# Performance work log

Hardware: AMD Instinct MI355X
Metric: run time of the kernel (lower is better)

The kernel has to match this reference:

```python
import jax, jax.numpy as jnp
import numpy as np

DIM = 1024
HEADS = 16
HEAD_DIM = DIM // HEADS
SCALE = HEAD_DIM ** -0.5


def setup_inputs() -> dict:
    key = jax.random.key(0)
    ks = jax.random.split(key, 9)
    b, n, m = 4, 1024, 1024
    x = jax.random.normal(ks[0], (b, n, DIM), dtype=jnp.float32)
    context = jax.random.normal(ks[1], (b, m, DIM), dtype=jnp.float32)
    mask = jax.random.randint(ks[2], (b, n, 32, 32), 0, 2, dtype=jnp.int32)
    s = DIM ** -0.5
    Wq = jax.random.normal(ks[3], (DIM, DIM), dtype=jnp.float32) * s
    bq = jnp.zeros((DIM,), dtype=jnp.float32)
    Wkv = jax.random.normal(ks[4], (DIM, 2 * DIM), dtype=jnp.float32) * s
    bkv = jnp.zeros((2 * DIM,), dtype=jnp.float32)
    Wp = jax.random.normal(ks[5], (DIM, DIM), dtype=jnp.float32) * s
    bp = jnp.zeros((DIM,), dtype=jnp.float32)
    return {"x": x, "context": context, "mask": mask,
            "Wq": Wq, "bq": bq, "Wkv": Wkv, "bkv": bkv, "Wp": Wp, "bp": bp}


def reference(x, context, mask, Wq, bq, Wkv, bkv, Wp, bp):
    b, n, _ = x.shape
    m = context.shape[1]
    h, d = HEADS, HEAD_DIM
    # projections
    q = (x @ Wq + bq).reshape(b, n, h, d).transpose(0, 2, 1, 3)       # [b,h,n,d]
    kv = (context @ Wkv + bkv).reshape(b, m, 2, h, d)
    k = kv[:, :, 0].transpose(0, 2, 1, 3)                              # [b,h,m,d]
    v = kv[:, :, 1].transpose(0, 2, 1, 3)                              # [b,h,m,d]
    dots = jnp.einsum('bhnd,bhmd->bhnm', q, k) * SCALE                 # [b,h,n,m]
    # mask: [b,n,H,W] -> [b,1,n,m]; masked_fill where mask == 0
    mflat = mask.reshape(b, n, m)[:, None]                             # [b,1,n,m]
    dots = jnp.where(mflat == 0, -jnp.inf, dots)
    attn = jax.nn.softmax(dots, axis=-1)
    out = jnp.einsum('bhnm,bhmd->bhnd', attn, v)
    out = out.transpose(0, 2, 1, 3).reshape(b, n, h * d)
    return out @ Wp + bp
```

## Files before the change

kernel.cpp:

```cpp
#include <hip/hip_runtime.h>

typedef __bf16 bf16;
typedef __bf16 bf16x8 __attribute__((ext_vector_type(8)));
typedef __bf16 bf16x4 __attribute__((ext_vector_type(4)));
typedef float f32x4 __attribute__((ext_vector_type(4)));
typedef unsigned long long u64;

#define MFMA16(a, b, c) __builtin_amdgcn_mfma_f32_16x16x32_bf16(a, b, c, 0, 0, 0)

__device__ __forceinline__ void gl_lds16(const void* g, void* l) {
  __builtin_amdgcn_global_load_lds(
      (const __attribute__((address_space(1))) unsigned int*)g,
      (__attribute__((address_space(3))) unsigned int*)l, 16, 0, 0);
}

template <int N>
__device__ __forceinline__ void wait_vmcnt() {
  asm volatile("s_waitcnt vmcnt(%0)" ::"n"(N) : "memory");
}

__device__ __forceinline__ void bar() {
  asm volatile("" ::: "memory");
  __builtin_amdgcn_s_barrier();
  asm volatile("" ::: "memory");
}

__device__ __forceinline__ float hw_exp2(float x) {
#if __has_builtin(__builtin_amdgcn_exp2f)
  return __builtin_amdgcn_exp2f(x);
#else
  float r;
  asm("v_exp_f32 %0, %1" : "=v"(r) : "v"(x));
  return r;
#endif
}

__global__ __launch_bounds__(256)
void prep_k(const float* __restrict__ Wq, const float* __restrict__ Wkv,
            const float* __restrict__ Wp, const int* __restrict__ mask,
            const float* __restrict__ context, const float* __restrict__ x,
            bf16* __restrict__ BqkvT, bf16* __restrict__ WpT,
            u64* __restrict__ maskbits, bf16* __restrict__ cb,
            bf16* __restrict__ xb) {
  const int bx = blockIdx.x;
  const int tid = threadIdx.x;
  if (bx >= 3328) {
    const size_t i = ((size_t)(bx - 3328) * 256 + tid) * 8;
    f32x4 a0 = *(const f32x4*)(x + i);
    f32x4 a1 = *(const f32x4*)(x + i + 4);
    bf16x8 t;
#pragma unroll
    for (int j = 0; j < 4; ++j) { t[j] = (bf16)a0[j]; t[4 + j] = (bf16)a1[j]; }
    *(bf16x8*)(xb + i) = t;
    return;
  }
  if (bx >= 1280) {
    const size_t i = ((size_t)(bx - 1280) * 256 + tid) * 8;
    f32x4 a0 = *(const f32x4*)(context + i);
    f32x4 a1 = *(const f32x4*)(context + i + 4);
    bf16x8 t;
#pragma unroll
    for (int j = 0; j < 4; ++j) { t[j] = (bf16)a0[j]; t[4 + j] = (bf16)a1[j]; }
    *(bf16x8*)(cb + i) = t;
    return;
  }
  if (bx >= 1024) {
    const int idx = (bx - 1024) * 256 + tid;
    const int4* p = (const int4*)(mask + (size_t)idx * 64);
    u64 v = 0;
#pragma unroll
    for (int i = 0; i < 16; ++i) {
      int4 m = p[i];
      v |= (u64)(m.x != 0) << (4 * i);
      v |= (u64)(m.y != 0) << (4 * i + 1);
      v |= (u64)(m.z != 0) << (4 * i + 2);
      v |= (u64)(m.w != 0) << (4 * i + 3);
    }
    maskbits[idx] = v;
    return;
  }
  const int ct = bx >> 4, rt = bx & 15;
  const float* src;
  bf16* dst;
  int C, c0, drow0;
  if (ct < 16) {
    src = Wq; C = 1024; c0 = ct * 64; dst = BqkvT; drow0 = c0;
  } else if (ct < 48) {
    src = Wkv; C = 2048; c0 = (ct - 16) * 64; dst = BqkvT; drow0 = 1024 + c0;
  } else {
    src = Wp; C = 1024; c0 = (ct - 48) * 64; dst = WpT; drow0 = c0;
  }
  __shared__ bf16 T[64][72];
  const int r0 = rt * 64;
#pragma unroll
  for (int i = 0; i < 2; ++i) {
    int c = i * 256 + tid;
    int row = c >> 3, col = (c & 7) * 8;
    const float* sp = &src[(size_t)(r0 + row) * C + c0 + col];
    f32x4 a0 = *(const f32x4*)sp;
    f32x4 a1 = *(const f32x4*)(sp + 4);
    bf16x8 t;
#pragma unroll
    for (int j = 0; j < 4; ++j) { t[j] = (bf16)a0[j]; t[4 + j] = (bf16)a1[j]; }
    *(bf16x8*)&T[row][col] = t;
  }
  __syncthreads();
#pragma unroll
  for (int i = 0; i < 2; ++i) {
    int c = i * 256 + tid;
    int orow = c >> 3, ocol = (c & 7) * 8;
    bf16x8 v;
#pragma unroll
    for (int j = 0; j < 8; ++j) v[j] = T[ocol + j][orow];
    *(bf16x8*)&dst[(size_t)(drow0 + orow) * 1024 + r0 + ocol] = v;
  }
}

template <int EPI, int BN>
__global__ __launch_bounds__(256, BN == 128 ? 3 : 4)
void gemm_p3(const bf16* __restrict__ A0, const bf16* __restrict__ A1,
             const bf16* __restrict__ Bt, const float* __restrict__ bias0,
             const float* __restrict__ bias1, bf16* __restrict__ oq,
             bf16* __restrict__ ok, bf16* __restrict__ ovt,
             float* __restrict__ outf) {
  constexpr int NJ = BN / 32;
  constexpr int S = 2 + BN / 64;
  __shared__ bf16 As[3][128][32];
  __shared__ bf16 Bs[3][BN][32];
  const int tid = threadIdx.x;
  const int lane = tid & 63;
  const int w = tid >> 6;
  const int wm = (w >> 1) * 64;
  const int wn = (w & 1) * (BN / 2);
  const int l15 = lane & 15, l4 = lane >> 4;
  const int lrow = lane >> 2;
  const int lcg = (lane & 3) ^ ((lrow >> 1) & 3);
  const int rdc = (l4 ^ ((l15 >> 1) & 3)) * 8;
  const int m0 = blockIdx.x * 128;
  const int n0 = blockIdx.y * BN;

  const bf16* Asrc = (EPI == 1) ? ((n0 < 1024) ? A0 : A1) : A0;

  float bc[NJ];
#pragma unroll
  for (int j = 0; j < NJ; ++j) {
    const int col = n0 + wn + j * 16 + l15;
    if (EPI == 1) bc[j] = (col < 1024) ? bias0[col] : bias1[col - 1024];
    else bc[j] = bias0[col];
  }

  f32x4 acc[4][NJ] = {};

#define STAGE(kk, buf)                                                        \
  {                                                                           \
    _Pragma("unroll") for (int it = 0; it < 2; ++it) {                        \
      const int r = w * 32 + it * 16;                                         \
      gl_lds16(&Asrc[(size_t)(m0 + r + lrow) * 1024 + (kk) + lcg * 8],        \
               &As[buf][r][0]);                                               \
    }                                                                         \
    _Pragma("unroll") for (int it = 0; it < BN / 64; ++it) {                  \
      const int r = w * (BN / 4) + it * 16;                                   \
      gl_lds16(&Bt[(size_t)(n0 + r + lrow) * 1024 + (kk) + lcg * 8],          \
               &Bs[buf][r][0]);                                               \
    }                                                                         \
  }

#define COMPUTE(buf)                                                          \
  {                                                                           \
    bf16x8 af[4], bfr[NJ];                                                    \
    _Pragma("unroll") for (int i = 0; i < 4; ++i) af[i] =                     \
        *(const bf16x8*)&As[buf][wm + i * 16 + l15][rdc];                     \
    _Pragma("unroll") for (int j = 0; j < NJ; ++j) bfr[j] =                   \
        *(const bf16x8*)&Bs[buf][wn + j * 16 + l15][rdc];                     \
    _Pragma("unroll") for (int i = 0; i < 4; ++i)                             \
        _Pragma("unroll") for (int j = 0; j < NJ; ++j) acc[i][j] =            \
            MFMA16(af[i], bfr[j], acc[i][j]);                                 \
  }

  STAGE(0, 0);
  STAGE(32, 1);
#pragma unroll 3
  for (int k = 0; k < 30; ++k) {
    wait_vmcnt<S>();
    bar();
    STAGE((k + 2) * 32, (k + 2) % 3);
    COMPUTE(k % 3);
  }
  wait_vmcnt<S>();
  bar();
  COMPUTE(0);
  wait_vmcnt<0>();
  bar();
  COMPUTE(1);
#undef STAGE
#undef COMPUTE

  const float SCALE2 = 0.18033688011112042f;
#pragma unroll
  for (int j = 0; j < NJ; ++j) {
    const int col = n0 + wn + j * 16 + l15;
#pragma unroll
    for (int i = 0; i < 4; ++i) {
#pragma unroll
      for (int r = 0; r < 4; ++r) {
        const int row = m0 + wm + i * 16 + l4 * 4 + r;
        const float v = acc[i][j][r] + bc[j];
        if (EPI == 0) {
          outf[(size_t)row * 1024 + col] = v;
        } else {
          const int b = row >> 10, n = row & 1023;
          if (col < 1024) {
            const int h = col >> 6, d = col & 63;
            oq[(((size_t)(b * 16 + h)) * 1024 + n) * 64 + d] =
                (bf16)(v * SCALE2);
          } else {
            const int ckv = col - 1024;
            const int s = ckv >> 10, c2 = ckv & 1023;
            const int h = c2 >> 6, d = c2 & 63;
            if (s == 0)
              ok[(((size_t)(b * 16 + h)) * 1024 + n) * 64 + d] = (bf16)v;
            else
              ovt[(((size_t)(b * 16 + h)) * 64 + d) * 1024 + n] = (bf16)v;
          }
        }
      }
    }
  }
}

__global__ __launch_bounds__(256, 2)
void attn_kernel(const bf16* __restrict__ q, const bf16* __restrict__ k,
                 const bf16* __restrict__ vT, const u64* __restrict__ maskbits,
                 bf16* __restrict__ ao) {
  const int bh = blockIdx.x;
  const int ntile = blockIdx.y;
  const int b = bh >> 4, h = bh & 15;
  const int tid = threadIdx.x;
  const int lane = tid & 63;
  const int w = tid >> 6;
  const int l15 = lane & 15, l4 = lane >> 4;

  __shared__ bf16 Ks[2][64][64];
  __shared__ bf16 Vts[2][64][64];
  __shared__ bf16 Pw[4][32][64];

  const size_t base = (size_t)bh * 65536;
  const int nrow0 = ntile * 128 + w * 32;

  bf16x8 qf[2][2];
#pragma unroll
  for (int f = 0; f < 2; ++f)
#pragma unroll
    for (int ks = 0; ks < 2; ++ks)
      qf[f][ks] = *(const bf16x8*)&q[base +
                                     (size_t)(nrow0 + f * 16 + l15) * 64 +
                                     ks * 32 + l4 * 8];

  const u64* mb = maskbits + (size_t)(b * 1024 + nrow0 + l15) * 16;

  const int srow = lane >> 3;
  const int sgl = (lane & 7) ^ srow;
  const bf16* kp = &k[base + (size_t)(w * 16 + srow) * 64 + sgl * 8];
  const bf16* vp = &vT[base + (size_t)(w * 16 + srow) * 1024 + sgl * 8];

  const int rc0 = ((0 + l4) ^ (l15 & 7)) * 8;
  const int rc1 = ((4 + l4) ^ (l15 & 7)) * 8;

  const int sh0 = l4 * 4;
  const int sh1 = 16 + l4 * 4;

  f32x4 o[2][4] = {};
  float lsum[2] = {0.0f, 0.0f};

#define STAGEA(mt_, buf_)                                                     \
  {                                                                           \
    _Pragma("unroll") for (int it = 0; it < 2; ++it) {                        \
      gl_lds16(kp + (size_t)((mt_)*64 + it * 8) * 64,                         \
               &Ks[buf_][w * 16 + it * 8][0]);                                \
      gl_lds16(vp + (size_t)(it * 8) * 1024 + (mt_)*64,                       \
               &Vts[buf_][w * 16 + it * 8][0]);                               \
    }                                                                         \
  }

  STAGEA(0, 0);
  u64 wm0 = mb[0];
  u64 wm1 = mb[256];
  for (int mt = 0; mt < 16; ++mt) {
    const int cur = mt & 1;
    __syncthreads();
    if (mt < 15) STAGEA(mt + 1, cur ^ 1);
    u64 nm0 = 0, nm1 = 0;
    if (mt < 15) {
      nm0 = mb[mt + 1];
      nm1 = mb[256 + mt + 1];
    }

    f32x4 s[2][4];
    __builtin_amdgcn_s_setprio(1);
#pragma unroll
    for (int sub = 0; sub < 4; ++sub) {
      bf16x8 kf0 = *(const bf16x8*)&Ks[cur][sub * 16 + l15][rc0];
      bf16x8 kf1 = *(const bf16x8*)&Ks[cur][sub * 16 + l15][rc1];
      s[0][sub] = MFMA16(kf0, qf[0][0], (f32x4)0.0f);
      s[0][sub] = MFMA16(kf1, qf[0][1], s[0][sub]);
      s[1][sub] = MFMA16(kf0, qf[1][0], (f32x4)0.0f);
      s[1][sub] = MFMA16(kf1, qf[1][1], s[1][sub]);
    }
    __builtin_amdgcn_s_setprio(0);

#pragma unroll
    for (int f = 0; f < 2; ++f) {
      const u64 wmt = f ? wm1 : wm0;
      const unsigned mlo = (unsigned)wmt;
      const unsigned mhi = (unsigned)(wmt >> 32);
#pragma unroll
      for (int sub = 0; sub < 4; ++sub) {
        const unsigned word = (sub < 2) ? mlo : mhi;
        const unsigned nib = (word >> ((sub & 1) ? sh1 : sh0)) & 15u;
        float p[4];
#pragma unroll
        for (int r = 0; r < 4; ++r) {
          float e = hw_exp2(s[f][sub][r]);
          p[r] = ((nib >> r) & 1u) ? e : 0.0f;
        }
        lsum[f] += (p[0] + p[1]) + (p[2] + p[3]);
        bf16x4 pv;
#pragma unroll
        for (int r = 0; r < 4; ++r) pv[r] = (bf16)p[r];
        const int gw = sub * 2 + (l4 >> 1);
        char* pd = (char*)&Pw[w][f * 16 + l15][0] +
                   ((gw ^ (l15 & 7)) * 16 + (l4 & 1) * 8);
        *(bf16x4*)pd = pv;
      }
    }

    bf16x8 af[2][2];
#pragma unroll
    for (int f = 0; f < 2; ++f) {
      af[f][0] = *(const bf16x8*)&Pw[w][f * 16 + l15][rc0];
      af[f][1] = *(const bf16x8*)&Pw[w][f * 16 + l15][rc1];
    }
    __builtin_amdgcn_s_setprio(1);
#pragma unroll
    for (int sub = 0; sub < 4; ++sub) {
      bf16x8 vf0 = *(const bf16x8*)&Vts[cur][sub * 16 + l15][rc0];
      bf16x8 vf1 = *(const bf16x8*)&Vts[cur][sub * 16 + l15][rc1];
      o[0][sub] = MFMA16(af[0][0], vf0, o[0][sub]);
      o[0][sub] = MFMA16(af[0][1], vf1, o[0][sub]);
      o[1][sub] = MFMA16(af[1][0], vf0, o[1][sub]);
      o[1][sub] = MFMA16(af[1][1], vf1, o[1][sub]);
    }
    __builtin_amdgcn_s_setprio(0);

    wm0 = nm0;
    wm1 = nm1;
  }
#undef STAGEA

  float inv[2][4];
#pragma unroll
  for (int f = 0; f < 2; ++f) {
    float t = lsum[f];
    t += __shfl_xor(t, 16);
    t += __shfl_xor(t, 32);
#pragma unroll
    for (int r = 0; r < 4; ++r) inv[f][r] = 1.0f / __shfl(t, l4 * 4 + r);
  }

#pragma unroll
  for (int f = 0; f < 2; ++f) {
#pragma unroll
    for (int sub = 0; sub < 4; ++sub) {
#pragma unroll
      for (int r = 0; r < 4; ++r) {
        const int n = nrow0 + f * 16 + l4 * 4 + r;
        const size_t idx =
            ((size_t)(b * 1024 + n)) * 1024 + h * 64 + sub * 16 + l15;
        ao[idx] = (bf16)(o[f][sub][r] * inv[f][r]);
      }
    }
  }
}

extern "C" void kernel_launch(void* const* d_in, const int* in_sizes, int n_in,
                              void* d_out, int out_size, void* d_ws,
                              size_t ws_size, hipStream_t stream) {
  const float* x = (const float*)d_in[0];
  const float* context = (const float*)d_in[1];
  const int* mask = (const int*)d_in[2];
  const float* Wq = (const float*)d_in[3];
  const float* bq = (const float*)d_in[4];
  const float* Wkv = (const float*)d_in[5];
  const float* bkv = (const float*)d_in[6];
  const float* Wp = (const float*)d_in[7];
  const float* bp = (const float*)d_in[8];
  float* out = (float*)d_out;

  char* ws = (char*)d_ws;
  bf16* cb = (bf16*)(ws);
  bf16* aow = (bf16*)(ws);
  bf16* xb = (bf16*)(ws + (8ull << 20));
  bf16* BqkvT = (bf16*)(ws + (16ull << 20));
  bf16* qw = (bf16*)(ws + (22ull << 20));
  bf16* kw = (bf16*)(ws + (30ull << 20));
  bf16* vtw = (bf16*)(ws + (38ull << 20));
  u64* maskbits = (u64*)(ws + (46ull << 20));
  bf16* WpT = (bf16*)(ws + (46ull << 20) + (512ull << 10));

  const dim3 blk(256);

  prep_k<<<dim3(5376), blk, 0, stream>>>(Wq, Wkv, Wp, mask, context, x, BqkvT,
                                         WpT, maskbits, cb, xb);

  gemm_p3<1, 128><<<dim3(32, 24), blk, 0, stream>>>(xb, cb, BqkvT, bq, bkv,
                                                    qw, kw, vtw, nullptr);

  attn_kernel<<<dim3(64, 8), blk, 0, stream>>>(qw, kw, vtw, maskbits, aow);

  gemm_p3<0, 64><<<dim3(32, 16), blk, 0, stream>>>(aow, nullptr, WpT, bp,
                                                   nullptr, nullptr, nullptr,
                                                   nullptr, out);
}
```

Baseline: 205.0 us.

## Fuse fp32-to-bf16 conversion of x and context into QKV GEMM

Removes the separate prep pass that converted x and context to bf16 in workspace. A new QKV GEMM kernel instead loads the fp32 activation tiles straight into shared memory with a swizzled layout and converts them to bf16 while building the MFMA fragments. This avoids a round trip of 32 MB through global memory, at the cost of loading fp32 A tiles, which doubles A-side load bandwidth and LDS footprint. Pipelining drops to a two-buffer scheme.

```diff
diff --git a/kernel.cpp b/kernel.cpp
--- a/kernel.cpp
+++ b/kernel.cpp
@@ -38,32 +38,10 @@
 __global__ __launch_bounds__(256)
 void prep_k(const float* __restrict__ Wq, const float* __restrict__ Wkv,
             const float* __restrict__ Wp, const int* __restrict__ mask,
-            const float* __restrict__ context, const float* __restrict__ x,
             bf16* __restrict__ BqkvT, bf16* __restrict__ WpT,
-            u64* __restrict__ maskbits, bf16* __restrict__ cb,
-            bf16* __restrict__ xb) {
+            u64* __restrict__ maskbits) {
   const int bx = blockIdx.x;
   const int tid = threadIdx.x;
-  if (bx >= 3328) {
-    const size_t i = ((size_t)(bx - 3328) * 256 + tid) * 8;
-    f32x4 a0 = *(const f32x4*)(x + i);
-    f32x4 a1 = *(const f32x4*)(x + i + 4);
-    bf16x8 t;
-#pragma unroll
-    for (int j = 0; j < 4; ++j) { t[j] = (bf16)a0[j]; t[4 + j] = (bf16)a1[j]; }
-    *(bf16x8*)(xb + i) = t;
-    return;
-  }
-  if (bx >= 1280) {
-    const size_t i = ((size_t)(bx - 1280) * 256 + tid) * 8;
-    f32x4 a0 = *(const f32x4*)(context + i);
-    f32x4 a1 = *(const f32x4*)(context + i + 4);
-    bf16x8 t;
-#pragma unroll
-    for (int j = 0; j < 4; ++j) { t[j] = (bf16)a0[j]; t[4 + j] = (bf16)a1[j]; }
-    *(bf16x8*)(cb + i) = t;
-    return;
-  }
   if (bx >= 1024) {
     const int idx = (bx - 1024) * 256 + tid;
     const int4* p = (const int4*)(mask + (size_t)idx * 64);
@@ -113,6 +91,114 @@
 #pragma unroll
     for (int j = 0; j < 8; ++j) v[j] = T[ocol + j][orow];
     *(bf16x8*)&dst[(size_t)(drow0 + orow) * 1024 + r0 + ocol] = v;
+  }
+}
+
+__global__ __launch_bounds__(256, 3)
+void gemm_qkvf(const float* __restrict__ x, const float* __restrict__ ctx,
+               const bf16* __restrict__ Bt, const float* __restrict__ bq,
+               const float* __restrict__ bkv, bf16* __restrict__ oq,
+               bf16* __restrict__ ok, bf16* __restrict__ ovt) {
+  __shared__ float Asf[2][128][32];
+  __shared__ bf16 Bs[2][128][32];
+  const int tid = threadIdx.x;
+  const int lane = tid & 63;
+  const int w = tid >> 6;
+  const int wm = (w >> 1) * 64;
+  const int wn = (w & 1) * 64;
+  const int l15 = lane & 15, l4 = lane >> 4;
+  const int lrow = lane >> 2;
+  const int lcg = (lane & 3) ^ ((lrow >> 1) & 3);
+  const int rdc = (l4 ^ ((l15 >> 1) & 3)) * 8;
+  const int arow = lane >> 3;
+  const int alg = (lane & 7) ^ arow;
+  const int s7 = l15 & 7;
+  const int m0 = blockIdx.x * 128;
+  const int n0 = blockIdx.y * 128;
+
+  const float* Af = (n0 < 1024) ? x : ctx;
+
+  float bc[4];
+#pragma unroll
+  for (int j = 0; j < 4; ++j) {
+    const int col = n0 + wn + j * 16 + l15;
+    bc[j] = (col < 1024) ? bq[col] : bkv[col - 1024];
+  }
+
+  f32x4 acc[4][4] = {};
+
+#define STAGE(kk, buf)                                                        \
+  {                                                                           \
+    _Pragma("unroll") for (int it = 0; it < 4; ++it) {                        \
+      const int rb = w * 32 + it * 8;                                         \
+      gl_lds16(&Af[(size_t)(m0 + rb + arow) * 1024 + (kk) + alg * 4],         \
+               &Asf[buf][rb][0]);                                             \
+    }                                                                         \
+    _Pragma("unroll") for (int it = 0; it < 2; ++it) {                        \
+      const int r = w * 32 + it * 16;                                         \
+      gl_lds16(&Bt[(size_t)(n0 + r + lrow) * 1024 + (kk) + lcg * 8],          \
+               &Bs[buf][r][0]);                                               \
+    }                                                                         \
+  }
+
+#define COMPUTE(buf)                                                          \
+  {                                                                           \
+    bf16x8 af[4], bfr[4];                                                     \
+    _Pragma("unroll") for (int i = 0; i < 4; ++i) {                           \
+      const float* ap = &Asf[buf][wm + i * 16 + l15][0];                      \
+      f32x4 a0 = *(const f32x4*)(ap + (((2 * l4) ^ s7) * 4));                 \
+      f32x4 a1 = *(const f32x4*)(ap + (((2 * l4 + 1) ^ s7) * 4));             \
+      bf16x8 t;                                                               \
+      _Pragma("unroll") for (int u = 0; u < 4; ++u) {                         \
+        t[u] = (bf16)a0[u];                                                   \
+        t[4 + u] = (bf16)a1[u];                                               \
+      }                                                                       \
+      af[i] = t;                                                              \
+    }                                                                         \
+    _Pragma("unroll") for (int j = 0; j < 4; ++j) bfr[j] =                    \
+        *(const bf16x8*)&Bs[buf][wn + j * 16 + l15][rdc];                     \
+    _Pragma("unroll") for (int i = 0; i < 4; ++i)                             \
+        _Pragma("unroll") for (int j = 0; j < 4; ++j) acc[i][j] =             \
+            MFMA16(af[i], bfr[j], acc[i][j]);                                 \
+  }
+
+  STAGE(0, 0);
+  for (int k = 0; k < 32; k += 2) {
+    __syncthreads();
+    STAGE((k + 1) * 32, 1);
+    COMPUTE(0);
+    __syncthreads();
+    if (k < 30) STAGE((k + 2) * 32, 0);
+    COMPUTE(1);
+  }
+#undef STAGE
+#undef COMPUTE
+
+  const float SCALE2 = 0.18033688011112042f;
+#pragma unroll
+  for (int j = 0; j < 4; ++j) {
+    const int col = n0 + wn + j * 16 + l15;
+#pragma unroll
+    for (int i = 0; i < 4; ++i) {
+#pragma unroll
+      for (int r = 0; r < 4; ++r) {
+        const int row = m0 + wm + i * 16 + l4 * 4 + r;
+        const float v = acc[i][j][r] + bc[j];
+        const int b = row >> 10, n = row & 1023;
+        if (col < 1024) {
+          const int h = col >> 6, d = col & 63;
+          oq[(((size_t)(b * 16 + h)) * 1024 + n) * 64 + d] = (bf16)(v * SCALE2);
+        } else {
+          const int ckv = col - 1024;
+          const int s = ckv >> 10, c2 = ckv & 1023;
+          const int h = c2 >> 6, d = c2 & 63;
+          if (s == 0)
+            ok[(((size_t)(b * 16 + h)) * 1024 + n) * 64 + d] = (bf16)v;
+          else
+            ovt[(((size_t)(b * 16 + h)) * 64 + d) * 1024 + n] = (bf16)v;
+        }
+      }
+    }
   }
 }
 
@@ -397,23 +483,21 @@
   float* out = (float*)d_out;
 
   char* ws = (char*)d_ws;
-  bf16* cb = (bf16*)(ws);
   bf16* aow = (bf16*)(ws);
-  bf16* xb = (bf16*)(ws + (8ull << 20));
-  bf16* BqkvT = (bf16*)(ws + (16ull << 20));
-  bf16* qw = (bf16*)(ws + (22ull << 20));
-  bf16* kw = (bf16*)(ws + (30ull << 20));
-  bf16* vtw = (bf16*)(ws + (38ull << 20));
-  u64* maskbits = (u64*)(ws + (46ull << 20));
-  bf16* WpT = (bf16*)(ws + (46ull << 20) + (512ull << 10));
+  bf16* BqkvT = (bf16*)(ws + (8ull << 20));
+  bf16* qw = (bf16*)(ws + (14ull << 20));
+  bf16* kw = (bf16*)(ws + (22ull << 20));
+  bf16* vtw = (bf16*)(ws + (30ull << 20));
+  u64* maskbits = (u64*)(ws + (38ull << 20));
+  bf16* WpT = (bf16*)(ws + (38ull << 20) + (512ull << 10));
 
   const dim3 blk(256);
 
-  prep_k<<<dim3(5376), blk, 0, stream>>>(Wq, Wkv, Wp, mask, context, x, BqkvT,
-                                         WpT, maskbits, cb, xb);
-
-  gemm_p3<1, 128><<<dim3(32, 24), blk, 0, stream>>>(xb, cb, BqkvT, bq, bkv,
-                                                    qw, kw, vtw, nullptr);
+  prep_k<<<dim3(1280), blk, 0, stream>>>(Wq, Wkv, Wp, mask, BqkvT, WpT,
+                                         maskbits);
+
+  gemm_qkvf<<<dim3(32, 24), blk, 0, stream>>>(x, context, BqkvT, bq, bkv,
+                                              qw, kw, vtw);
 
   attn_kernel<<<dim3(64, 8), blk, 0, stream>>>(qw, kw, vtw, maskbits, aow);
 
```

Measured after the change: 218.7 us. 1.07x slower.
